# Optimization experiments

Measured on AMD Instinct MI355X. Metric: run time of the kernel, lower is better.

## Reference

```python
import jax, jax.numpy as jnp
import numpy as np

M, N = 128, 128          # SOM grid
NITER = 1000             # total training iterations
ALPHA = 0.3              # base learning rate (torch default)
SIGMA = max(M, N) / 2.0  # base neighbourhood radius (torch default)
BS, DIM = 4096, 768


def setup_inputs() -> dict:
    key = jax.random.key(0)
    k1, k2 = jax.random.split(key)
    embedded = jax.random.normal(k1, (BS, DIM), dtype=jnp.float32)   # SapBERT CLS reps
    weights = jax.random.normal(k2, (M * N, DIM), dtype=jnp.float32)  # codebook / SOM weights
    return {"embedded": embedded, "weights": weights, "it": 100}


def reference(embedded, weights, it):
    comps = weights.shape[0]
    # neuron grid locations [comps, 2] (row-major i,j like neuron_locations())
    locs = jnp.stack(
        jnp.meshgrid(jnp.arange(M), jnp.arange(N), indexing="ij"), axis=-1
    ).reshape(comps, 2).astype(jnp.float32)

    # BMU search: squared Euclidean distances (argmin identical to argmin of sqrt)
    # [bs, comps] — avoids materializing the torch [bs, comps, dim] repeat
    d2 = (
        jnp.sum(embedded * embedded, axis=1)[:, None]
        + jnp.sum(weights * weights, axis=1)[None, :]
        - 2.0 * (embedded @ weights.T)
    )
    bmu_index = jnp.argmin(d2, axis=1)          # [bs]
    bmu_loc = locs[bmu_index]                   # [bs, 2] gather

    # linearly decaying learning rate / sigma
    decay = 1.0 - it / NITER
    alpha_op = ALPHA * decay
    sigma_op = SIGMA * decay

    # Gaussian neighbourhood over grid distances [bs, comps]
    grid_d2 = jnp.sum((locs[None, :, :] - bmu_loc[:, None, :]) ** 2, axis=-1)
    lr = alpha_op * jnp.exp(-grid_d2 / (sigma_op * sigma_op))

    # delta[c,d] = sum_b lr[b,c] * (x[b,d] - w[c,d])  (no bs x comps x dim materialization)
    delta = jnp.einsum("bc,bd->cd", lr, embedded) - jnp.sum(lr, axis=0)[:, None] * weights
    return weights + delta
```

## Files before the change

### kernel.cpp

```cpp
#include <hip/hip_runtime.h>
#include <cstdint>
#include <cstddef>

#define BS    4096
#define DIM   768
#define GM    128
#define GN    128
#define COMPS (GM * GN)
#define NITER_F 1000.0f
#define ALPHA0  0.3f
#define SIGMA0  64.0f

typedef _Float16 half8  __attribute__((ext_vector_type(8)));
typedef _Float16 half4v __attribute__((ext_vector_type(4)));
typedef float    floatx4 __attribute__((ext_vector_type(4)));

#define XH_OFF    0UL
#define WH_OFF    (8UL * 1024UL * 1024UL)
#define G_OFF     0UL
#define G_BYTES   ((size_t)COMPS * DIM * 4UL)
#define BEST_OFF  G_BYTES
#define BEST_BYTES ((size_t)BS * 8UL)
#define CNT_OFF   (BEST_OFF + BEST_BYTES)
#define CNT_BYTES ((size_t)COMPS * 4UL)
#define WN2_OFF   (CNT_OFF + CNT_BYTES)

#define GPTR(p) ((const __attribute__((address_space(1))) void*)(p))
#define LPTR(p) ((__attribute__((address_space(3))) void*)(p))

__device__ __forceinline__ unsigned long long packScore(float s, int c) {
    unsigned u = __float_as_uint(s);
    u = (u & 0x80000000u) ? ~u : (u | 0x80000000u);
    return ((unsigned long long)u << 32) | (unsigned)(~(unsigned)c);
}

__device__ __forceinline__ unsigned long long shfl_xor_u64(unsigned long long v, int m) {
    unsigned lo = (unsigned)v, hi = (unsigned)(v >> 32);
    lo = (unsigned)__shfl_xor((int)lo, m, 64);
    hi = (unsigned)__shfl_xor((int)hi, m, 64);
    return ((unsigned long long)hi << 32) | lo;
}

__global__ void cvt_kernel(const float* __restrict__ src, _Float16* __restrict__ dst, int n4) {
    int i = blockIdx.x * 256 + threadIdx.x;
    if (i >= n4) return;
    float4 v = ((const float4*)src)[i];
    half4v h;
    h[0] = (_Float16)v.x; h[1] = (_Float16)v.y;
    h[2] = (_Float16)v.z; h[3] = (_Float16)v.w;
    ((half4v*)dst)[i] = h;
}

__global__ __launch_bounds__(192) void cvtw_wn2_kernel(
    const float* __restrict__ w, _Float16* __restrict__ wh, float* __restrict__ wn2) {
    const int c = blockIdx.x;
    const int t = threadIdx.x;
    const size_t i4 = (size_t)c * 192 + t;
    float4 v = ((const float4*)w)[i4];
    half4v h;
    h[0] = (_Float16)v.x; h[1] = (_Float16)v.y;
    h[2] = (_Float16)v.z; h[3] = (_Float16)v.w;
    ((half4v*)wh)[i4] = h;
    float s = v.x * v.x + v.y * v.y + v.z * v.z + v.w * v.w;
    #pragma unroll
    for (int off = 32; off; off >>= 1) s += __shfl_down(s, off, 64);
    __shared__ float p[3];
    if ((t & 63) == 0) p[t >> 6] = s;
    __syncthreads();
    if (t == 0) wn2[c] = 0.5f * (p[0] + p[1] + p[2]);
}

__global__ __launch_bounds__(256) void bmu_kernel(
    const _Float16* __restrict__ xh, const _Float16* __restrict__ wh,
    const float* __restrict__ wn2, unsigned long long* __restrict__ best) {
    __shared__ _Float16 xs[128 * 64];
    __shared__ _Float16 wsd[128 * 64];
    __shared__ unsigned long long red[128];

    const int tid  = threadIdx.x;
    const int wv   = tid >> 6;
    const int lane = tid & 63;
    const int c0 = blockIdx.x * 128;
    const int b0 = blockIdx.y * 128;

    if (tid < 128) red[tid] = 0ULL;

    floatx4 acc[4][4];
    #pragma unroll
    for (int i = 0; i < 4; ++i)
        #pragma unroll
        for (int j = 0; j < 4; ++j) acc[i][j] = (floatx4){0.f, 0.f, 0.f, 0.f};

    const int srow = lane >> 3;
    const int spos = lane & 7;
    const int q    = lane >> 4;
    const int l15  = lane & 15;
    const int mrow = (wv >> 1) * 64;
    const int ncol = (wv & 1) * 64;

    for (int k0 = 0; k0 < DIM; k0 += 64) {
        #pragma unroll
        for (int s = 0; s < 4; ++s) {
            const int rbase = wv * 32 + s * 8;
            const int row = rbase + srow;
            const int kk = spos ^ (row & 7);
            const _Float16* gx = xh + (size_t)(b0 + row) * DIM + k0 + kk * 8;
            __builtin_amdgcn_global_load_lds(GPTR(gx), LPTR(xs + rbase * 64), 16, 0, 0);
            const _Float16* gw = wh + (size_t)(c0 + row) * DIM + k0 + kk * 8;
            __builtin_amdgcn_global_load_lds(GPTR(gw), LPTR(wsd + rbase * 64), 16, 0, 0);
        }
        __syncthreads();

        #pragma unroll
        for (int h = 0; h < 2; ++h) {
            half8 af[4], bf[4];
            #pragma unroll
            for (int i = 0; i < 4; ++i) {
                const int row = mrow + i * 16 + l15;
                const int ck = (h * 4 + q) ^ (row & 7);
                af[i] = *(const half8*)(xs + row * 64 + ck * 8);
            }
            #pragma unroll
            for (int j = 0; j < 4; ++j) {
                const int row = ncol + j * 16 + l15;
                const int ck = (h * 4 + q) ^ (row & 7);
                bf[j] = *(const half8*)(wsd + row * 64 + ck * 8);
            }
            #pragma unroll
            for (int i = 0; i < 4; ++i)
                #pragma unroll
                for (int j = 0; j < 4; ++j)
                    acc[i][j] = __builtin_amdgcn_mfma_f32_16x16x32_f16(af[i], bf[j], acc[i][j], 0, 0, 0);
        }
        __syncthreads();
    }

    float wnj[4];
    #pragma unroll
    for (int j = 0; j < 4; ++j) wnj[j] = wn2[c0 + ncol + j * 16 + l15];

    #pragma unroll
    for (int i = 0; i < 4; ++i) {
        #pragma unroll
        for (int r = 0; r < 4; ++r) {
            unsigned long long m = 0ULL;
            #pragma unroll
            for (int j = 0; j < 4; ++j) {
                float s = acc[i][j][r] - wnj[j];
                unsigned long long p = packScore(s, c0 + ncol + j * 16 + l15);
                if (p > m) m = p;
            }
            #pragma unroll
            for (int msk = 1; msk <= 8; msk <<= 1) {
                unsigned long long o = shfl_xor_u64(m, msk);
                if (o > m) m = o;
            }
            if (l15 == 0)
                atomicMax(&red[mrow + i * 16 + q * 4 + r], m);
        }
    }
    __syncthreads();
    if (tid < 128) atomicMax(&best[b0 + tid], red[tid]);
}

__global__ void scatter_kernel(const unsigned long long* __restrict__ best,
                               const float* __restrict__ x,
                               float* __restrict__ G, float* __restrict__ cnt) {
    const int b = blockIdx.x;
    const int c = (int)(~(unsigned)(best[b] & 0xFFFFFFFFULL));
    float* gr = G + (size_t)c * DIM;
    const float* xr = x + (size_t)b * DIM;
    #pragma unroll
    for (int u = 0; u < 3; ++u) {
        const int d = threadIdx.x + u * 256;
        atomicAdd(&gr[d], xr[d]);
    }
    if (threadIdx.x == 0) atomicAdd(&cnt[c], 1.0f);
}

#define EP 136
#define BP 40

__global__ __launch_bounds__(256) void convA_kernel(
    const float* G, _Float16* Hh, const int* __restrict__ itp) {
    __shared__ _Float16 Es[128 * EP];
    __shared__ _Float16 Bs[128 * BP];
    const int d0 = blockIdx.x * 128;
    const int ib = blockIdx.y;
    const int tid = threadIdx.x;
    const int wv = tid >> 6, lane = tid & 63;
    const int l15 = lane & 15, q = lane >> 4;
    const int mrow = (wv >> 1) * 64, ncol = (wv & 1) * 64;

    {
        const float decay = 1.f - (float)(*itp) / NITER_F;
        const float sig = SIGMA0 * decay;
        const float inv = -1.f / (sig * sig);
        const int row = tid >> 1, hh = tid & 1;
        _Float16* dst = Es + row * EP + hh * 64;
        #pragma unroll
        for (int u = 0; u < 64; ++u) {
            const float dd = (float)(row - hh * 64 - u);
            dst[u] = (_Float16)__expf(dd * dd * inv);
        }
    }

    floatx4 acc[4][4];
    #pragma unroll
    for (int i = 0; i < 4; ++i)
        #pragma unroll
        for (int j = 0; j < 4; ++j) acc[i][j] = (floatx4){0.f, 0.f, 0.f, 0.f};

    const int dpo = (tid & 15) * 8;
    const int rsel = tid >> 4;
    for (int k0 = 0; k0 < 128; k0 += 32) {
        __syncthreads();
        #pragma unroll
        for (int s = 0; s < 2; ++s) {
            const int j = k0 + s * 16 + rsel;
            const float* r = G + (size_t)(ib * 128 + j) * DIM + d0 + dpo;
            float4 a0 = *(const float4*)r, a1 = *(const float4*)(r + 4);
            float va[8] = {a0.x, a0.y, a0.z, a0.w, a1.x, a1.y, a1.z, a1.w};
            #pragma unroll
            for (int u = 0; u < 8; ++u)
                Bs[(dpo + u) * BP + (s * 16 + rsel)] = (_Float16)va[u];
        }
        __syncthreads();
        half8 af[4], bf[4];
        #pragma unroll
        for (int i = 0; i < 4; ++i)
            af[i] = *(const half8*)(Es + (mrow + i * 16 + l15) * EP + k0 + q * 8);
        #pragma unroll
        for (int j = 0; j < 4; ++j)
            bf[j] = *(const half8*)(Bs + (ncol + j * 16 + l15) * BP + q * 8);
        #pragma unroll
        for (int i = 0; i < 4; ++i)
            #pragma unroll
            for (int j = 0; j < 4; ++j)
                acc[i][j] = __builtin_amdgcn_mfma_f32_16x16x32_f16(af[i], bf[j], acc[i][j], 0, 0, 0);
    }
    __syncthreads();
    float* Ebf = (float*)Es;
    #pragma unroll
    for (int ch = 0; ch < 2; ++ch) {
        if ((wv >> 1) == ch) {
            #pragma unroll
            for (int i = 0; i < 4; ++i)
                #pragma unroll
                for (int j = 0; j < 4; ++j)
                    #pragma unroll
                    for (int r = 0; r < 4; ++r)
                        Ebf[(i * 16 + q * 4 + r) * 132 + ncol + j * 16 + l15] = acc[i][j][r];
        }
        __syncthreads();
        {
            const int row = tid >> 2, seg = tid & 3;
            const int m = ch * 64 + row;
            _Float16* hp = Hh + (size_t)(ib * 128 + m) * 1536 + d0 * 2 + seg * 32;
            #pragma unroll
            for (int u = 0; u < 4; ++u) {
                const float* sp = Ebf + row * 132 + seg * 32 + u * 8;
                half8 hv;
                #pragma unroll
                for (int e = 0; e < 8; ++e) hv[e] = (_Float16)sp[e];
                *(half8*)(hp + u * 8) = hv;
            }
        }
        __syncthreads();
    }
}

__global__ __launch_bounds__(256) void convB_kernel(
    const _Float16* Hh, const float* __restrict__ w, const float* __restrict__ cnt,
    const int* __restrict__ itp, float* __restrict__ out) {
    __shared__ _Float16 Es[128 * EP];
    __shared__ _Float16 Bs[128 * BP];
    __shared__ float cntHs[128];
    __shared__ float Ss[128];
    const int d0 = blockIdx.x * 128;
    const int jc = blockIdx.y;
    const int tid = threadIdx.x;
    const int wv = tid >> 6, lane = tid & 63;
    const int l15 = lane & 15, q = lane >> 4;
    const int mrow = (wv >> 1) * 64, ncol = (wv & 1) * 64;
    const float decay = 1.f - (float)(*itp) / NITER_F;
    const float alpha = ALPHA0 * decay;
    const float sig = SIGMA0 * decay;
    const float inv = -1.f / (sig * sig);

    if (tid < 128) {
        float s = 0.f;
        for (int j = 0; j < 128; ++j) {
            const float dd = (float)(jc - j);
            s += __expf(dd * dd * inv) * cnt[tid * 128 + j];
        }
        cntHs[tid] = s;
    }
    {
        const int row = tid >> 1, hh = tid & 1;
        _Float16* dst = Es + row * EP + hh * 64;
        #pragma unroll
        for (int u = 0; u < 64; ++u) {
            const float dd = (float)(row - hh * 64 - u);
            dst[u] = (_Float16)__expf(dd * dd * inv);
        }
    }
    __syncthreads();
    if (tid < 128) {
        float s = 0.f;
        for (int i = 0; i < 128; ++i) {
            const float dd = (float)(tid - i);
            s += __expf(dd * dd * inv) * cntHs[i];
        }
        Ss[tid] = s;
    }

    floatx4 acc[4][4];
    #pragma unroll
    for (int i = 0; i < 4; ++i)
        #pragma unroll
        for (int j = 0; j < 4; ++j) acc[i][j] = (floatx4){0.f, 0.f, 0.f, 0.f};

    const int dpo = (tid & 15) * 8;
    const int rsel = tid >> 4;
    for (int k0 = 0; k0 < 128; k0 += 32) {
        __syncthreads();
        #pragma unroll
        for (int s = 0; s < 2; ++s) {
            const int i = k0 + s * 16 + rsel;
            const half8 v = *(const half8*)(Hh + (size_t)(i * 128 + jc) * 1536 + d0 * 2 + dpo);
            #pragma unroll
            for (int u = 0; u < 8; ++u)
                Bs[(dpo + u) * BP + (s * 16 + rsel)] = v[u];
        }
        __syncthreads();
        half8 af[4], bf[4];
        #pragma unroll
        for (int i = 0; i < 4; ++i)
            af[i] = *(const half8*)(Es + (mrow + i * 16 + l15) * EP + k0 + q * 8);
        #pragma unroll
        for (int j = 0; j < 4; ++j)
            bf[j] = *(const half8*)(Bs + (ncol + j * 16 + l15) * BP + q * 8);
        #pragma unroll
        for (int i = 0; i < 4; ++i)
            #pragma unroll
            for (int j = 0; j < 4; ++j)
                acc[i][j] = __builtin_amdgcn_mfma_f32_16x16x32_f16(af[i], bf[j], acc[i][j], 0, 0, 0);
    }
    __syncthreads();
    float* Ebf = (float*)Es;
    #pragma unroll
    for (int ch = 0; ch < 2; ++ch) {
        if ((wv >> 1) == ch) {
            #pragma unroll
            for (int i = 0; i < 4; ++i)
                #pragma unroll
                for (int j = 0; j < 4; ++j)
                    #pragma unroll
                    for (int r = 0; r < 4; ++r)
                        Ebf[(i * 16 + q * 4 + r) * 132 + ncol + j * 16 + l15] = acc[i][j][r];
        }
        __syncthreads();
        {
            const int row = tid >> 2, seg = tid & 3;
            const int m = ch * 64 + row;
            const int c = m * 128 + jc;
            const float scl = 1.f - alpha * Ss[m];
            const size_t g = (size_t)c * DIM + d0 + seg * 32;
            #pragma unroll
            for (int u = 0; u < 8; ++u) {
                float4 wv4 = *(const float4*)(w + g + u * 4);
                float4 t4  = *(const float4*)(Ebf + row * 132 + seg * 32 + u * 4);
                float4 o;
                o.x = wv4.x * scl + alpha * t4.x;
                o.y = wv4.y * scl + alpha * t4.y;
                o.z = wv4.z * scl + alpha * t4.z;
                o.w = wv4.w * scl + alpha * t4.w;
                *(float4*)(out + g + u * 4) = o;
            }
        }
        __syncthreads();
    }
}

extern "C" void kernel_launch(void* const* d_in, const int* in_sizes, int n_in,
                              void* d_out, int out_size, void* d_ws, size_t ws_size,
                              hipStream_t stream) {
    const float* x  = (const float*)d_in[0];
    const float* w  = (const float*)d_in[1];
    const int* itp  = (const int*)d_in[2];
    float* out = (float*)d_out;
    char* ws = (char*)d_ws;

    _Float16* xh = (_Float16*)(ws + XH_OFF);
    _Float16* wh = (_Float16*)(ws + WH_OFF);
    float*    G  = (float*)(ws + G_OFF);
    _Float16* Hh = (_Float16*)(ws + G_OFF);
    unsigned long long* best = (unsigned long long*)(ws + BEST_OFF);
    float* cnt  = (float*)(ws + CNT_OFF);
    float* wn2  = (float*)(ws + WN2_OFF);

    hipMemsetAsync(ws + BEST_OFF, 0, BEST_BYTES + CNT_BYTES, stream);

    cvt_kernel<<<(BS * DIM / 4 + 255) / 256, 256, 0, stream>>>(x, xh, BS * DIM / 4);
    cvtw_wn2_kernel<<<COMPS, 192, 0, stream>>>(w, wh, wn2);

    bmu_kernel<<<dim3(COMPS / 128, BS / 128), 256, 0, stream>>>(xh, wh, wn2, best);

    hipMemsetAsync(ws + G_OFF, 0, G_BYTES, stream);
    scatter_kernel<<<BS, 256, 0, stream>>>(best, x, G, cnt);

    convA_kernel<<<dim3(6, 128), 256, 0, stream>>>(G, Hh, itp);
    convB_kernel<<<dim3(6, 128), 256, 0, stream>>>(Hh, w, cnt, itp, out);
}
```

Baseline: 367.0 us.

## Rewrite BMU GEMM with 256x256 tiles, 4-stage LDS pipeline and XCD-aware mapping

The BMU distance GEMM moves from 128x128 tiles with a single LDS buffer and two barriers per K step to 256x256 tiles with 512 threads. K tiles of 32 rotate through four LDS buffers, with three tiles kept in flight. Global-to-LDS loads for later stages are interleaved between MFMA groups, and s_setprio raises priority around the MFMAs. Blocks are remapped so each XCD handles a contiguous range of codebook columns for L2 reuse. The cost is many more accumulator registers per thread and a much larger LDS footprint, which can reduce occupancy.

```diff
diff --git a/kernel.cpp b/kernel.cpp
--- a/kernel.cpp
+++ b/kernel.cpp
@@ -70,97 +70,158 @@
     if (t == 0) wn2[c] = 0.5f * (p[0] + p[1] + p[2]);
 }
 
-__global__ __launch_bounds__(256) void bmu_kernel(
+#define BMU_NT 24
+
+__global__ __launch_bounds__(512, 2) void bmu_kernel(
     const _Float16* __restrict__ xh, const _Float16* __restrict__ wh,
     const float* __restrict__ wn2, unsigned long long* __restrict__ best) {
-    __shared__ _Float16 xs[128 * 64];
-    __shared__ _Float16 wsd[128 * 64];
-    __shared__ unsigned long long red[128];
+    __shared__ _Float16 AB[4][2][8192];
+    __shared__ unsigned long long red[256];
 
     const int tid  = threadIdx.x;
     const int wv   = tid >> 6;
     const int lane = tid & 63;
-    const int c0 = blockIdx.x * 128;
-    const int b0 = blockIdx.y * 128;
-
-    if (tid < 128) red[tid] = 0ULL;
-
-    floatx4 acc[4][4];
-    #pragma unroll
-    for (int i = 0; i < 4; ++i)
-        #pragma unroll
-        for (int j = 0; j < 4; ++j) acc[i][j] = (floatx4){0.f, 0.f, 0.f, 0.f};
-
-    const int srow = lane >> 3;
-    const int spos = lane & 7;
+    const int l15  = lane & 15;
     const int q    = lane >> 4;
-    const int l15  = lane & 15;
-    const int mrow = (wv >> 1) * 64;
-    const int ncol = (wv & 1) * 64;
-
-    for (int k0 = 0; k0 < DIM; k0 += 64) {
-        #pragma unroll
-        for (int s = 0; s < 4; ++s) {
-            const int rbase = wv * 32 + s * 8;
-            const int row = rbase + srow;
-            const int kk = spos ^ (row & 7);
-            const _Float16* gx = xh + (size_t)(b0 + row) * DIM + k0 + kk * 8;
-            __builtin_amdgcn_global_load_lds(GPTR(gx), LPTR(xs + rbase * 64), 16, 0, 0);
-            const _Float16* gw = wh + (size_t)(c0 + row) * DIM + k0 + kk * 8;
-            __builtin_amdgcn_global_load_lds(GPTR(gw), LPTR(wsd + rbase * 64), 16, 0, 0);
-        }
-        __syncthreads();
-
-        #pragma unroll
-        for (int h = 0; h < 2; ++h) {
-            half8 af[4], bf[4];
-            #pragma unroll
-            for (int i = 0; i < 4; ++i) {
-                const int row = mrow + i * 16 + l15;
-                const int ck = (h * 4 + q) ^ (row & 7);
-                af[i] = *(const half8*)(xs + row * 64 + ck * 8);
-            }
-            #pragma unroll
-            for (int j = 0; j < 4; ++j) {
-                const int row = ncol + j * 16 + l15;
-                const int ck = (h * 4 + q) ^ (row & 7);
-                bf[j] = *(const half8*)(wsd + row * 64 + ck * 8);
-            }
-            #pragma unroll
-            for (int i = 0; i < 4; ++i)
-                #pragma unroll
-                for (int j = 0; j < 4; ++j)
-                    acc[i][j] = __builtin_amdgcn_mfma_f32_16x16x32_f16(af[i], bf[j], acc[i][j], 0, 0, 0);
-        }
-        __syncthreads();
+    const int wr   = wv >> 2;
+    const int wc   = wv & 3;
+
+    const int bid = blockIdx.x;
+    const int xcd = bid & 7;
+    const int rem = bid >> 3;
+    const int bb  = rem & 15;
+    const int cb  = xcd * 8 + (rem >> 4);
+    const int b0 = bb * 256;
+    const int c0 = cb * 256;
+
+    if (tid < 256) red[tid] = 0ULL;
+
+    const int Ls = tid >> 3;
+    const int ss = tid & 7;
+    const int sl = ss ^ (Ls & 7);
+    const int prow = 2 * Ls + (sl >> 2);
+    const int kc8  = (sl & 3) * 8;
+    const _Float16* gA0 = xh + (size_t)(b0 + prow) * DIM + kc8;
+    const _Float16* gA1 = gA0 + (size_t)128 * DIM;
+    const _Float16* gB0 = wh + (size_t)(c0 + prow) * DIM + kc8;
+    const _Float16* gB1 = gB0 + (size_t)128 * DIM;
+    const int ldsoff = wv * 512;
+
+    int aoff[8], boff[4];
+    #pragma unroll
+    for (int i = 0; i < 8; ++i) {
+        const int row = wr * 128 + i * 16 + l15;
+        const int line = row >> 1;
+        const int ps = (((row & 1) << 2) | q) ^ (line & 7);
+        aoff[i] = line * 64 + ps * 8;
+    }
+    #pragma unroll
+    for (int jj = 0; jj < 4; ++jj) {
+        const int row = wc * 64 + jj * 16 + l15;
+        const int line = row >> 1;
+        const int ps = (((row & 1) << 2) | q) ^ (line & 7);
+        boff[jj] = line * 64 + ps * 8;
+    }
+
+    floatx4 acc[8][4];
+    #pragma unroll
+    for (int i = 0; i < 8; ++i)
+        #pragma unroll
+        for (int jj = 0; jj < 4; ++jj) acc[i][jj] = (floatx4){0.f, 0.f, 0.f, 0.f};
+
+    #pragma unroll
+    for (int t = 0; t < 3; ++t) {
+        _Float16* A = &AB[t][0][0];
+        _Float16* B = &AB[t][1][0];
+        __builtin_amdgcn_global_load_lds(GPTR(gA0 + t * 32), LPTR(A + ldsoff),        16, 0, 0);
+        __builtin_amdgcn_global_load_lds(GPTR(gA1 + t * 32), LPTR(A + 4096 + ldsoff), 16, 0, 0);
+        __builtin_amdgcn_global_load_lds(GPTR(gB0 + t * 32), LPTR(B + ldsoff),        16, 0, 0);
+        __builtin_amdgcn_global_load_lds(GPTR(gB1 + t * 32), LPTR(B + 4096 + ldsoff), 16, 0, 0);
+    }
+
+    for (int t = 0; t < BMU_NT; ++t) {
+        if (t < BMU_NT - 2)       asm volatile("s_waitcnt vmcnt(8)" ::: "memory");
+        else if (t == BMU_NT - 2) asm volatile("s_waitcnt vmcnt(4)" ::: "memory");
+        else                      asm volatile("s_waitcnt vmcnt(0)" ::: "memory");
+        __builtin_amdgcn_s_barrier();
+        asm volatile("" ::: "memory");
+
+        const _Float16* A = &AB[t & 3][0][0];
+        const _Float16* B = &AB[t & 3][1][0];
+        const bool more = (t + 3) < BMU_NT;
+        _Float16* An = &AB[(t + 3) & 3][0][0];
+        _Float16* Bn = &AB[(t + 3) & 3][1][0];
+        const int t3 = (t + 3) * 32;
+
+        half8 af[8], bf[4];
+        #pragma unroll
+        for (int i = 0; i < 4; ++i) af[i] = *(const half8*)(A + aoff[i]);
+        bf[0] = *(const half8*)(B + boff[0]);
+        bf[1] = *(const half8*)(B + boff[1]);
+        if (more) __builtin_amdgcn_global_load_lds(GPTR(gA0 + t3), LPTR(An + ldsoff), 16, 0, 0);
+        __builtin_amdgcn_s_setprio(1);
+        #pragma unroll
+        for (int i = 0; i < 4; ++i) {
+            acc[i][0] = __builtin_amdgcn_mfma_f32_16x16x32_f16(af[i], bf[0], acc[i][0], 0, 0, 0);
+            acc[i][1] = __builtin_amdgcn_mfma_f32_16x16x32_f16(af[i], bf[1], acc[i][1], 0, 0, 0);
+        }
+        __builtin_amdgcn_s_setprio(0);
+        #pragma unroll
+        for (int i = 4; i < 8; ++i) af[i] = *(const half8*)(A + aoff[i]);
+        if (more) __builtin_amdgcn_global_load_lds(GPTR(gA1 + t3), LPTR(An + 4096 + ldsoff), 16, 0, 0);
+        __builtin_amdgcn_s_setprio(1);
+        #pragma unroll
+        for (int i = 4; i < 8; ++i) {
+            acc[i][0] = __builtin_amdgcn_mfma_f32_16x16x32_f16(af[i], bf[0], acc[i][0], 0, 0, 0);
+            acc[i][1] = __builtin_amdgcn_mfma_f32_16x16x32_f16(af[i], bf[1], acc[i][1], 0, 0, 0);
+        }
+        __builtin_amdgcn_s_setprio(0);
+        bf[2] = *(const half8*)(B + boff[2]);
+        bf[3] = *(const half8*)(B + boff[3]);
+        if (more) __builtin_amdgcn_global_load_lds(GPTR(gB0 + t3), LPTR(Bn + ldsoff), 16, 0, 0);
+        __builtin_amdgcn_s_setprio(1);
+        #pragma unroll
+        for (int i = 4; i < 8; ++i) {
+            acc[i][2] = __builtin_amdgcn_mfma_f32_16x16x32_f16(af[i], bf[2], acc[i][2], 0, 0, 0);
+            acc[i][3] = __builtin_amdgcn_mfma_f32_16x16x32_f16(af[i], bf[3], acc[i][3], 0, 0, 0);
+        }
+        __builtin_amdgcn_s_setprio(0);
+        if (more) __builtin_amdgcn_global_load_lds(GPTR(gB1 + t3), LPTR(Bn + 4096 + ldsoff), 16, 0, 0);
+        __builtin_amdgcn_s_setprio(1);
+        #pragma unroll
+        for (int i = 0; i < 4; ++i) {
+            acc[i][2] = __builtin_amdgcn_mfma_f32_16x16x32_f16(af[i], bf[2], acc[i][2], 0, 0, 0);
+            acc[i][3] = __builtin_amdgcn_mfma_f32_16x16x32_f16(af[i], bf[3], acc[i][3], 0, 0, 0);
+        }
+        __builtin_amdgcn_s_setprio(0);
     }
 
     float wnj[4];
     #pragma unroll
-    for (int j = 0; j < 4; ++j) wnj[j] = wn2[c0 + ncol + j * 16 + l15];
-
-    #pragma unroll
-    for (int i = 0; i < 4; ++i) {
+    for (int jj = 0; jj < 4; ++jj) wnj[jj] = wn2[c0 + wc * 64 + jj * 16 + l15];
+
+    #pragma unroll
+    for (int i = 0; i < 8; ++i) {
         #pragma unroll
         for (int r = 0; r < 4; ++r) {
             unsigned long long m = 0ULL;
             #pragma unroll
-            for (int j = 0; j < 4; ++j) {
-                float s = acc[i][j][r] - wnj[j];
-                unsigned long long p = packScore(s, c0 + ncol + j * 16 + l15);
+            for (int jj = 0; jj < 4; ++jj) {
+                const float s = acc[i][jj][r] - wnj[jj];
+                const unsigned long long p = packScore(s, c0 + wc * 64 + jj * 16 + l15);
                 if (p > m) m = p;
             }
             #pragma unroll
             for (int msk = 1; msk <= 8; msk <<= 1) {
-                unsigned long long o = shfl_xor_u64(m, msk);
+                const unsigned long long o = shfl_xor_u64(m, msk);
                 if (o > m) m = o;
             }
             if (l15 == 0)
-                atomicMax(&red[mrow + i * 16 + q * 4 + r], m);
+                atomicMax(&red[wr * 128 + i * 16 + q * 4 + r], m);
         }
     }
     __syncthreads();
-    if (tid < 128) atomicMax(&best[b0 + tid], red[tid]);
+    if (tid < 256) atomicMax(&best[b0 + tid], red[tid]);
 }
 
 __global__ void scatter_kernel(const unsigned long long* __restrict__ best,
@@ -405,7 +466,7 @@
     cvt_kernel<<<(BS * DIM / 4 + 255) / 256, 256, 0, stream>>>(x, xh, BS * DIM / 4);
     cvtw_wn2_kernel<<<COMPS, 192, 0, stream>>>(w, wh, wn2);
 
-    bmu_kernel<<<dim3(COMPS / 128, BS / 128), 256, 0, stream>>>(xh, wh, wn2, best);
+    bmu_kernel<<<dim3(1024), 512, 0, stream>>>(xh, wh, wn2, best);
 
     hipMemsetAsync(ws + G_OFF, 0, G_BYTES, stream);
     scatter_kernel<<<BS, 256, 0, stream>>>(best, x, G, cnt);
```

Measured after the change: 332.2 us. -9.5%, faster.
